# Kernel tuning notes

Measured on AMD Instinct MI355X. Metric: run time of the kernel, lower is better.

## Reference

```python
import jax, jax.numpy as jnp
import numpy as np

D_MODEL = 1024
N_HEADS = 16
D_K = D_MODEL // N_HEADS


def setup_inputs() -> dict:
    key = jax.random.key(0)
    kx, kq, kk, kv, ko = jax.random.split(key, 5)
    scale = 1.0 / np.sqrt(D_MODEL)
    return {
        "x": jax.random.normal(kx, (2, 2048, D_MODEL), dtype=jnp.float32),
        "W_Q": jax.random.normal(kq, (D_MODEL, D_MODEL), dtype=jnp.float32) * scale,
        "W_K": jax.random.normal(kk, (D_MODEL, D_MODEL), dtype=jnp.float32) * scale,
        "W_V": jax.random.normal(kv, (D_MODEL, D_MODEL), dtype=jnp.float32) * scale,
        "W_O": jax.random.normal(ko, (D_MODEL, D_MODEL), dtype=jnp.float32) * scale,
    }


def reference(x, W_Q, W_K, W_V, W_O) -> jnp.ndarray:
    B, S, _ = x.shape
    # Projections; weights stored as (d_model, d_model), applied as x @ W (Linear weight transposed convention folded into init)
    def heads(w):
        return jnp.einsum('bsd,de->bse', x, w).reshape(B, S, N_HEADS, D_K).transpose(0, 2, 1, 3)
    Q, K, V = heads(W_Q), heads(W_K), heads(W_V)  # (B,H,S,d_k)
    scores = jnp.einsum('bhqd,bhkd->bhqk', Q, K) / jnp.sqrt(jnp.asarray(D_K, x.dtype))
    causal_mask = jnp.triu(jnp.ones((S, S), dtype=bool), k=1)  # True above diagonal
    scores = jnp.where(causal_mask[None, None], jnp.asarray(-jnp.inf, x.dtype), scores)
    attn = jax.nn.softmax(scores, axis=-1)
    out = jnp.einsum('bhqk,bhkd->bhqd', attn, V)  # (B,H,S,d_k)
    out = out.transpose(0, 2, 1, 3).reshape(B, S, N_HEADS * D_K)
    return jnp.einsum('bsd,de->bse', out, W_O)
```

## Files before the change

kernel.cpp:

```cpp
#include <hip/hip_runtime.h>

typedef unsigned short u16;
typedef unsigned int u32;
typedef __attribute__((ext_vector_type(8))) __bf16 bf16x8;
typedef __attribute__((ext_vector_type(2))) __bf16 bf16x2;
typedef __attribute__((ext_vector_type(4))) float f32x4;
typedef __attribute__((ext_vector_type(16))) float f32x16;
typedef __attribute__((ext_vector_type(4))) u32 u32x4;

__device__ inline u16 f2bf(float f) {
  unsigned u = __builtin_bit_cast(unsigned, f);
  u += 0x7FFFu + ((u >> 16) & 1u);
  return (u16)(u >> 16);
}

__device__ inline u32 packbf(float a, float b) {
  bf16x2 t;
  t[0] = (__bf16)a;
  t[1] = (__bf16)b;
  return __builtin_bit_cast(u32, t);
}

__device__ inline void async16(const void* g, void* l) {
  __builtin_amdgcn_global_load_lds((const __attribute__((address_space(1))) void*)g,
                                   (__attribute__((address_space(3))) void*)l, 16, 0, 0);
}

__global__ __launch_bounds__(256) void xconv(const float* __restrict__ x, u16* __restrict__ xb) {
  int i = blockIdx.x * 256 + threadIdx.x;
  float4 v = ((const float4*)x)[i];
  ushort4 r;
  r.x = f2bf(v.x); r.y = f2bf(v.y); r.z = f2bf(v.z); r.w = f2bf(v.w);
  ((ushort4*)xb)[i] = r;
}

__global__ __launch_bounds__(256) void wtrans4(const float* __restrict__ W0,
                                               const float* __restrict__ W1,
                                               const float* __restrict__ W2,
                                               const float* __restrict__ W3,
                                               u16* __restrict__ WtQKV,
                                               u16* __restrict__ WtO) {
  __shared__ u16 tile[32][33];
  const int z = blockIdx.z;
  const float* W = (z == 0) ? W0 : (z == 1) ? W1 : (z == 2) ? W2 : W3;
  u16* Wt = (z < 3) ? (WtQKV + (size_t)z * 1024 * 1024) : WtO;
  const float s = (z == 0) ? 0.18033688011112042f : 1.0f;
  const int e0 = blockIdx.x * 32;
  const int d0 = blockIdx.y * 32;
  const int tx = threadIdx.x & 31;
  const int ty = threadIdx.x >> 5;
#pragma unroll
  for (int i = ty; i < 32; i += 8)
    tile[i][tx] = f2bf(W[(size_t)(d0 + i) * 1024 + e0 + tx] * s);
  __syncthreads();
#pragma unroll
  for (int i = ty; i < 32; i += 8)
    Wt[(size_t)(e0 + i) * 1024 + d0 + tx] = tile[tx][i];
}

__global__ __launch_bounds__(256) void vtrans(const u16* __restrict__ QKV, u16* __restrict__ Vtg) {
  __shared__ u16 t[32][66];
  const int tid = threadIdx.x;
  const int s0 = blockIdx.x * 32, dg0 = blockIdx.y * 64, b = blockIdx.z;
  {
    const int i = tid >> 3, c = (tid & 7) * 8;
    uint4 v = *(const uint4*)(QKV + (size_t)(b * 2048 + s0 + i) * 3072 + 2048 + dg0 + c);
    u16 tmp[8];
    *(uint4*)tmp = v;
#pragma unroll
    for (int e = 0; e < 8; ++e) t[i][c + e] = tmp[e];
  }
  __syncthreads();
  {
    const int r = tid >> 2, cg = (tid & 3) * 8;
    u16 tmp[8];
#pragma unroll
    for (int e = 0; e < 8; ++e) tmp[e] = t[cg + e][r];
    *(uint4*)(Vtg + (size_t)(b * 1024 + dg0 + r) * 2048 + s0 + cg) = *(uint4*)tmp;
  }
}

template <int OUT_BF16>
__global__ __launch_bounds__(256) void gemm_bt(const u16* __restrict__ A,
                                               const u16* __restrict__ Bt,
                                               void* __restrict__ Cp,
                                               int M, int N, int K) {
  __shared__ __align__(16) u16 As[128 * 32];
  __shared__ __align__(16) u16 Bs[128 * 32];
  const int tid = threadIdx.x;
  const int lane = tid & 63;
  const int wave = tid >> 6;
  const int lr = lane & 15;
  const int lk = (lane >> 4) * 8;
  const int wm = (wave >> 1) * 64;
  const int wn = (wave & 1) * 64;
  const int bm = blockIdx.x * 128;
  const int bn = blockIdx.y * 128;
  const int srow = lane >> 2;
  const int scol = (lane & 3) * 8;

  f32x4 acc[4][4] = {};

  for (int k0 = 0; k0 < K; k0 += 32) {
#pragma unroll
    for (int r = 0; r < 2; ++r) {
      const int chunk = r * 4 + wave;
      const int row = chunk * 16 + srow;
      async16(A + (size_t)(bm + row) * K + k0 + scol, &As[chunk * 512 + lane * 8]);
      async16(Bt + (size_t)(bn + row) * K + k0 + scol, &Bs[chunk * 512 + lane * 8]);
    }
    __syncthreads();
    bf16x8 a[4], b[4];
#pragma unroll
    for (int i = 0; i < 4; ++i) {
      a[i] = *(const bf16x8*)&As[(wm + i * 16 + lr) * 32 + lk];
      b[i] = *(const bf16x8*)&Bs[(wn + i * 16 + lr) * 32 + lk];
    }
#pragma unroll
    for (int mi = 0; mi < 4; ++mi)
#pragma unroll
      for (int ni = 0; ni < 4; ++ni)
        acc[mi][ni] = __builtin_amdgcn_mfma_f32_16x16x32_bf16(a[mi], b[ni], acc[mi][ni], 0, 0, 0);
    __syncthreads();
  }

#pragma unroll
  for (int mi = 0; mi < 4; ++mi) {
#pragma unroll
    for (int ni = 0; ni < 4; ++ni) {
      const int col = bn + wn + ni * 16 + lr;
#pragma unroll
      for (int j = 0; j < 4; ++j) {
        const int row = bm + wm + mi * 16 + (lane >> 4) * 4 + j;
        if (OUT_BF16)
          ((u16*)Cp)[(size_t)row * N + col] = f2bf(acc[mi][ni][j]);
        else
          ((float*)Cp)[(size_t)row * N + col] = acc[mi][ni][j];
      }
    }
  }
}

__global__ __launch_bounds__(256, 2) void attn_kernel(const u16* __restrict__ QKV,
                                                      const u16* __restrict__ Vtg,
                                                      u16* __restrict__ Opart,
                                                      float* __restrict__ Lpart) {
  constexpr int S = 2048, LD = 3072;
  constexpr float MFIX = 12.0f;
  __shared__ __align__(16) u16 Ks[2][64 * 64];
  __shared__ __align__(16) u16 Vs[2][64 * 64];

  const int g = 7 - (blockIdx.x >> 1);
  const int c = blockIdx.x & 1;
  const int bh = blockIdx.y;
  const int b = bh >> 4, h = bh & 15;
  const int tid = threadIdx.x, lane = tid & 63, w = tid >> 6;
  const int l31 = lane & 31, lh = lane >> 5;

  const int qbase = g * 256 + w * 64;
  const int ktlast = 4 * g + w;
  const int ktbeg = c * (2 * g + 2);
  const int ktend = (c + 1) * (2 * g + 2);

  bf16x8 qf[2][4];
#pragma unroll
  for (int qh = 0; qh < 2; ++qh) {
    const u16* qrow = QKV + (size_t)(b * S + qbase + qh * 32 + l31) * LD + h * 64;
#pragma unroll
    for (int cc = 0; cc < 4; ++cc) qf[qh][cc] = *(const bf16x8*)(qrow + cc * 16 + lh * 8);
  }

  const int c0 = tid, c1 = tid + 256;
  const int r0 = c0 >> 3, x0 = ((c0 & 7) ^ (r0 & 7)) << 3;
  const int r1 = c1 >> 3, x1 = ((c1 & 7) ^ (r1 & 7)) << 3;
  const u16* Kbase = QKV + (size_t)b * S * LD + 1024 + h * 64;
  const u16* Vbase = Vtg + (size_t)bh * 64 * 2048;

#define STAGE(buf, kt_)                                                          \
  do {                                                                           \
    async16(Kbase + (size_t)((kt_)*64 + r0) * LD + x0, &Ks[buf][c0 * 8]);        \
    async16(Kbase + (size_t)((kt_)*64 + r1) * LD + x1, &Ks[buf][c1 * 8]);        \
    async16(Vbase + (size_t)r0 * 2048 + (kt_)*64 + x0, &Vs[buf][c0 * 8]);        \
    async16(Vbase + (size_t)r1 * 2048 + (kt_)*64 + x1, &Vs[buf][c1 * 8]);        \
  } while (0)

  f32x16 o00 = {}, o01 = {}, o10 = {}, o11 = {};
  float l0 = 0.f, l1 = 0.f;

#define TREE16(dst, arr)                                                         \
  do {                                                                           \
    float v_[16];                                                                \
    _Pragma("unroll") for (int r_ = 0; r_ < 16; ++r_) v_[r_] = (arr)[r_];        \
    _Pragma("unroll") for (int s_ = 8; s_ >= 1; s_ >>= 1)                        \
      _Pragma("unroll") for (int r_ = 0; r_ < s_; ++r_) v_[r_] += v_[r_ + s_];   \
    dst += v_[0];                                                                \
  } while (0)

#define MAKE_PA(pa, pk, sw, q4)                                                  \
  bf16x8 pa;                                                                     \
  {                                                                              \
    u32x4 wv_;                                                                   \
    wv_[0] = lh ? (sw)[(q4) + 2] : (pk)[(q4) + 0];                               \
    wv_[1] = lh ? (sw)[(q4) + 3] : (pk)[(q4) + 1];                               \
    wv_[2] = lh ? (pk)[(q4) + 2] : (sw)[(q4) + 0];                               \
    wv_[3] = lh ? (pk)[(q4) + 3] : (sw)[(q4) + 1];                               \
    pa = __builtin_bit_cast(bf16x8, wv_);                                        \
  }

  STAGE(0, ktbeg);

  int cur = 0;
  for (int kt = ktbeg; kt < ktend; ++kt) {
    if (kt + 1 < ktend) {
      STAGE(cur ^ 1, kt + 1);
      asm volatile("s_waitcnt vmcnt(4)" ::: "memory");
    } else {
      asm volatile("s_waitcnt vmcnt(0)" ::: "memory");
    }
    __builtin_amdgcn_s_barrier();
    __builtin_amdgcn_sched_barrier(0);

    const bool active = (kt <= ktlast);
    if (active) {
      const bool full = (kt < ktlast);
      const u16* ks = Ks[cur];
      const u16* vs = Vs[cur];

      f32x16 t00 = {}, t10 = {}, t01 = {}, t11 = {};
      __builtin_amdgcn_s_setprio(1);
#pragma unroll
      for (int cc = 0; cc < 4; ++cc) {
        const int ci = 2 * cc + lh;
        const bf16x8 kf0 = *(const bf16x8*)&ks[l31 * 64 + ((ci ^ (l31 & 7)) << 3)];
        const bf16x8 kf1 = *(const bf16x8*)&ks[(32 + l31) * 64 + ((ci ^ (l31 & 7)) << 3)];
        t00 = __builtin_amdgcn_mfma_f32_32x32x16_bf16(kf0, qf[0][cc], t00, 0, 0, 0);
        t01 = __builtin_amdgcn_mfma_f32_32x32x16_bf16(kf0, qf[1][cc], t01, 0, 0, 0);
        if (full) t10 = __builtin_amdgcn_mfma_f32_32x32x16_bf16(kf1, qf[0][cc], t10, 0, 0, 0);
        t11 = __builtin_amdgcn_mfma_f32_32x32x16_bf16(kf1, qf[1][cc], t11, 0, 0, 0);
      }
      __builtin_amdgcn_s_setprio(0);

      if (!full) {
#pragma unroll
        for (int r = 0; r < 16; ++r) {
          const int ko = (r & 3) + 8 * (r >> 2) + 4 * lh;
          if (ko > l31) { t00[r] = -3e38f; t11[r] = -3e38f; }
        }
      }

      u32 pk0[8], pk1[8], sw0[8], sw1[8];

#pragma unroll
      for (int r = 0; r < 16; ++r) t00[r] = exp2f(t00[r] - MFIX);
#pragma unroll
      for (int r = 0; r < 16; ++r) t01[r] = exp2f(t01[r] - MFIX);
      TREE16(l0, t00);
      TREE16(l1, t01);
#pragma unroll
      for (int j = 0; j < 8; ++j) {
        pk0[j] = packbf(t00[2 * j], t00[2 * j + 1]);
        pk1[j] = packbf(t01[2 * j], t01[2 * j + 1]);
      }
#pragma unroll
      for (int j = 0; j < 8; ++j) {
        sw0[j] = __shfl_xor(pk0[j], 32);
        sw1[j] = __shfl_xor(pk1[j], 32);
      }
      __builtin_amdgcn_s_setprio(1);
#pragma unroll
      for (int kc = 0; kc < 2; ++kc) {
        const int q4 = kc * 4;
        MAKE_PA(pa0, pk0, sw0, q4)
        MAKE_PA(pa1, pk1, sw1, q4)
        const int ci = 2 * kc + lh;
        const bf16x8 vd0 = *(const bf16x8*)&vs[l31 * 64 + ((ci ^ (l31 & 7)) << 3)];
        const bf16x8 vd1 = *(const bf16x8*)&vs[(32 + l31) * 64 + ((ci ^ (l31 & 7)) << 3)];
        o00 = __builtin_amdgcn_mfma_f32_32x32x16_bf16(pa0, vd0, o00, 0, 0, 0);
        o01 = __builtin_amdgcn_mfma_f32_32x32x16_bf16(pa0, vd1, o01, 0, 0, 0);
        o10 = __builtin_amdgcn_mfma_f32_32x32x16_bf16(pa1, vd0, o10, 0, 0, 0);
        o11 = __builtin_amdgcn_mfma_f32_32x32x16_bf16(pa1, vd1, o11, 0, 0, 0);
      }
      __builtin_amdgcn_s_setprio(0);

      if (full) {
#pragma unroll
        for (int r = 0; r < 16; ++r) t10[r] = exp2f(t10[r] - MFIX);
        TREE16(l0, t10);
#pragma unroll
        for (int j = 0; j < 8; ++j) pk0[j] = packbf(t10[2 * j], t10[2 * j + 1]);
#pragma unroll
        for (int j = 0; j < 8; ++j) sw0[j] = __shfl_xor(pk0[j], 32);
      }
#pragma unroll
      for (int r = 0; r < 16; ++r) t11[r] = exp2f(t11[r] - MFIX);
      TREE16(l1, t11);
#pragma unroll
      for (int j = 0; j < 8; ++j) pk1[j] = packbf(t11[2 * j], t11[2 * j + 1]);
#pragma unroll
      for (int j = 0; j < 8; ++j) sw1[j] = __shfl_xor(pk1[j], 32);

      __builtin_amdgcn_s_setprio(1);
#pragma unroll
      for (int kc = 0; kc < 2; ++kc) {
        const int q4 = kc * 4;
        MAKE_PA(pa1, pk1, sw1, q4)
        const int ci = 2 * (kc + 2) + lh;
        const bf16x8 vd0 = *(const bf16x8*)&vs[l31 * 64 + ((ci ^ (l31 & 7)) << 3)];
        const bf16x8 vd1 = *(const bf16x8*)&vs[(32 + l31) * 64 + ((ci ^ (l31 & 7)) << 3)];
        if (full) {
          MAKE_PA(pa0, pk0, sw0, q4)
          o00 = __builtin_amdgcn_mfma_f32_32x32x16_bf16(pa0, vd0, o00, 0, 0, 0);
          o01 = __builtin_amdgcn_mfma_f32_32x32x16_bf16(pa0, vd1, o01, 0, 0, 0);
        }
        o10 = __builtin_amdgcn_mfma_f32_32x32x16_bf16(pa1, vd0, o10, 0, 0, 0);
        o11 = __builtin_amdgcn_mfma_f32_32x32x16_bf16(pa1, vd1, o11, 0, 0, 0);
      }
      __builtin_amdgcn_s_setprio(0);
    }

    asm volatile("s_waitcnt lgkmcnt(0)" ::: "memory");
    __builtin_amdgcn_s_barrier();
    cur ^= 1;
  }
#undef STAGE
#undef TREE16
#undef MAKE_PA

  const float l0t = l0 + __shfl_xor(l0, 32);
  const float l1t = l1 + __shfl_xor(l1, 32);
  u16* Oc = Opart + (size_t)c * 4096 * 1024;
#pragma unroll
  for (int r = 0; r < 16; ++r) {
    const int qo = (r & 3) + 8 * (r >> 2) + 4 * lh;
    u16* p0 = Oc + (size_t)(b * S + qbase + qo) * 1024 + h * 64 + l31;
    u16* p1 = p0 + (size_t)32 * 1024;
    p0[0] = f2bf(o00[r]);
    p0[32] = f2bf(o01[r]);
    p1[0] = f2bf(o10[r]);
    p1[32] = f2bf(o11[r]);
  }
  if (lh == 0) {
    Lpart[(size_t)c * 4096 * 16 + (size_t)(b * S + qbase + l31) * 16 + h] = l0t;
    Lpart[(size_t)c * 4096 * 16 + (size_t)(b * S + qbase + 32 + l31) * 16 + h] = l1t;
  }
}

__global__ __launch_bounds__(256) void combine(const u16* __restrict__ Opart,
                                               const float* __restrict__ Lpart,
                                               u16* __restrict__ Obuf) {
  const int i = blockIdx.x * 256 + threadIdx.x;
  const int row = i >> 7;
  const int cw = (i & 127) * 8;
  const int h = cw >> 6;
  const float l = Lpart[(size_t)row * 16 + h] + Lpart[(size_t)4096 * 16 + (size_t)row * 16 + h];
  const float inv = 1.0f / l;
  const bf16x8 a = *(const bf16x8*)(Opart + (size_t)row * 1024 + cw);
  const bf16x8 bq = *(const bf16x8*)(Opart + (size_t)4096 * 1024 + (size_t)row * 1024 + cw);
  u16 out[8];
#pragma unroll
  for (int j = 0; j < 8; ++j) out[j] = f2bf(((float)a[j] + (float)bq[j]) * inv);
  *(uint4*)(Obuf + (size_t)row * 1024 + cw) = *(uint4*)out;
}

extern "C" void kernel_launch(void* const* d_in, const int* in_sizes, int n_in,
                              void* d_out, int out_size, void* d_ws, size_t ws_size,
                              hipStream_t stream) {
  const float* x  = (const float*)d_in[0];
  const float* WQ = (const float*)d_in[1];
  const float* WK = (const float*)d_in[2];
  const float* WV = (const float*)d_in[3];
  const float* WO = (const float*)d_in[4];
  float* out = (float*)d_out;

  u16* xb    = (u16*)d_ws;
  u16* WtQKV = xb + (size_t)4096 * 1024;
  u16* WtO   = WtQKV + (size_t)3072 * 1024;
  u16* QKV   = WtO + (size_t)1024 * 1024;
  u16* Obuf  = QKV + (size_t)4096 * 3072;
  u16* Vtg   = Obuf + (size_t)4096 * 1024;
  u16* Opart = Vtg + (size_t)2048 * 2048;
  float* Lpart = (float*)(Opart + (size_t)2 * 4096 * 1024);

  xconv<<<4096, 256, 0, stream>>>(x, xb);
  wtrans4<<<dim3(32, 32, 4), 256, 0, stream>>>(WQ, WK, WV, WO, WtQKV, WtO);

  gemm_bt<1><<<dim3(32, 24), 256, 0, stream>>>(xb, WtQKV, QKV, 4096, 3072, 1024);
  vtrans<<<dim3(64, 16, 2), 256, 0, stream>>>(QKV, Vtg);
  attn_kernel<<<dim3(16, 32), 256, 0, stream>>>(QKV, Vtg, Opart, Lpart);
  combine<<<2048, 256, 0, stream>>>(Opart, Lpart, Obuf);
  gemm_bt<0><<<dim3(32, 8), 256, 0, stream>>>(Obuf, WtO, out, 4096, 1024, 1024);
}
```

Measured before the change: 147.5 us.

## Load V tiles directly into registers and drop the LDS V buffer

V tiles are no longer staged through shared memory. Each wave now loads its V fragments straight from global memory into a register double buffer (current and next tile), with the vmcnt wait adjusted so it retires only the current tile's loads. This halves LDS use, removes the V LDS reads, and raises the launch-bounds occupancy target from 2 to 3 blocks. In exchange, every wave re-fetches the same V tile from global/cache, and the extra register buffers under a tighter register budget risk spills or lower effective occupancy.

New measurement: 413.8 us. 2.81x slower.

```diff
diff --git a/kernel.cpp b/kernel.cpp
--- a/kernel.cpp
+++ b/kernel.cpp
@@ -141,14 +141,13 @@
   }
 }
 
-__global__ __launch_bounds__(256, 2) void attn_kernel(const u16* __restrict__ QKV,
+__global__ __launch_bounds__(256, 3) void attn_kernel(const u16* __restrict__ QKV,
                                                       const u16* __restrict__ Vtg,
                                                       u16* __restrict__ Opart,
                                                       float* __restrict__ Lpart) {
   constexpr int S = 2048, LD = 3072;
   constexpr float MFIX = 12.0f;
   __shared__ __align__(16) u16 Ks[2][64 * 64];
-  __shared__ __align__(16) u16 Vs[2][64 * 64];
 
   const int g = 7 - (blockIdx.x >> 1);
   const int c = blockIdx.x & 1;
@@ -174,14 +173,22 @@
   const int r0 = c0 >> 3, x0 = ((c0 & 7) ^ (r0 & 7)) << 3;
   const int r1 = c1 >> 3, x1 = ((c1 & 7) ^ (r1 & 7)) << 3;
   const u16* Kbase = QKV + (size_t)b * S * LD + 1024 + h * 64;
-  const u16* Vbase = Vtg + (size_t)bh * 64 * 2048;
-
-#define STAGE(buf, kt_)                                                          \
+  const u16* Vr0 = Vtg + (size_t)(bh * 64 + l31) * 2048;
+  const u16* Vr1 = Vtg + (size_t)(bh * 64 + 32 + l31) * 2048;
+
+#define STAGEK(buf, kt_)                                                         \
   do {                                                                           \
     async16(Kbase + (size_t)((kt_)*64 + r0) * LD + x0, &Ks[buf][c0 * 8]);        \
     async16(Kbase + (size_t)((kt_)*64 + r1) * LD + x1, &Ks[buf][c1 * 8]);        \
-    async16(Vbase + (size_t)r0 * 2048 + (kt_)*64 + x0, &Vs[buf][c0 * 8]);        \
-    async16(Vbase + (size_t)r1 * 2048 + (kt_)*64 + x1, &Vs[buf][c1 * 8]);        \
+  } while (0)
+
+#define VLOAD(d0_, d1_, kt_)                                                     \
+  do {                                                                           \
+    _Pragma("unroll") for (int kc = 0; kc < 4; ++kc) {                           \
+      const int ci = 2 * kc + lh;                                                \
+      d0_[kc] = *(const bf16x8*)(Vr0 + (kt_)*64 + ci * 8);                       \
+      d1_[kc] = *(const bf16x8*)(Vr1 + (kt_)*64 + ci * 8);                       \
+    }                                                                            \
   } while (0)
 
   f32x16 o00 = {}, o01 = {}, o10 = {}, o11 = {};
@@ -207,13 +214,18 @@
     pa = __builtin_bit_cast(bf16x8, wv_);                                        \
   }
 
-  STAGE(0, ktbeg);
+  bf16x8 vc0[4], vc1[4], vn0[4], vn1[4];
+
+  STAGEK(0, ktbeg);
+  VLOAD(vc0, vc1, ktbeg);
 
   int cur = 0;
   for (int kt = ktbeg; kt < ktend; ++kt) {
     if (kt + 1 < ktend) {
-      STAGE(cur ^ 1, kt + 1);
-      asm volatile("s_waitcnt vmcnt(4)" ::: "memory");
+      STAGEK(cur ^ 1, kt + 1);
+      VLOAD(vn0, vn1, kt + 1);
+      __builtin_amdgcn_sched_barrier(0);
+      asm volatile("s_waitcnt vmcnt(10)" ::: "memory");
     } else {
       asm volatile("s_waitcnt vmcnt(0)" ::: "memory");
     }
@@ -224,7 +236,6 @@
     if (active) {
       const bool full = (kt < ktlast);
       const u16* ks = Ks[cur];
-      const u16* vs = Vs[cur];
 
       f32x16 t00 = {}, t10 = {}, t01 = {}, t11 = {};
       __builtin_amdgcn_s_setprio(1);
@@ -272,13 +283,10 @@
         const int q4 = kc * 4;
         MAKE_PA(pa0, pk0, sw0, q4)
         MAKE_PA(pa1, pk1, sw1, q4)
-        const int ci = 2 * kc + lh;
-        const bf16x8 vd0 = *(const bf16x8*)&vs[l31 * 64 + ((ci ^ (l31 & 7)) << 3)];
-        const bf16x8 vd1 = *(const bf16x8*)&vs[(32 + l31) * 64 + ((ci ^ (l31 & 7)) << 3)];
-        o00 = __builtin_amdgcn_mfma_f32_32x32x16_bf16(pa0, vd0, o00, 0, 0, 0);
-        o01 = __builtin_amdgcn_mfma_f32_32x32x16_bf16(pa0, vd1, o01, 0, 0, 0);
-        o10 = __builtin_amdgcn_mfma_f32_32x32x16_bf16(pa1, vd0, o10, 0, 0, 0);
-        o11 = __builtin_amdgcn_mfma_f32_32x32x16_bf16(pa1, vd1, o11, 0, 0, 0);
+        o00 = __builtin_amdgcn_mfma_f32_32x32x16_bf16(pa0, vc0[kc], o00, 0, 0, 0);
+        o01 = __builtin_amdgcn_mfma_f32_32x32x16_bf16(pa0, vc1[kc], o01, 0, 0, 0);
+        o10 = __builtin_amdgcn_mfma_f32_32x32x16_bf16(pa1, vc0[kc], o10, 0, 0, 0);
+        o11 = __builtin_amdgcn_mfma_f32_32x32x16_bf16(pa1, vc1[kc], o11, 0, 0, 0);
       }
       __builtin_amdgcn_s_setprio(0);
 
@@ -304,25 +312,28 @@
       for (int kc = 0; kc < 2; ++kc) {
         const int q4 = kc * 4;
         MAKE_PA(pa1, pk1, sw1, q4)
-        const int ci = 2 * (kc + 2) + lh;
-        const bf16x8 vd0 = *(const bf16x8*)&vs[l31 * 64 + ((ci ^ (l31 & 7)) << 3)];
-        const bf16x8 vd1 = *(const bf16x8*)&vs[(32 + l31) * 64 + ((ci ^ (l31 & 7)) << 3)];
         if (full) {
           MAKE_PA(pa0, pk0, sw0, q4)
-          o00 = __builtin_amdgcn_mfma_f32_32x32x16_bf16(pa0, vd0, o00, 0, 0, 0);
-          o01 = __builtin_amdgcn_mfma_f32_32x32x16_bf16(pa0, vd1, o01, 0, 0, 0);
+          o00 = __builtin_amdgcn_mfma_f32_32x32x16_bf16(pa0, vc0[kc + 2], o00, 0, 0, 0);
+          o01 = __builtin_amdgcn_mfma_f32_32x32x16_bf16(pa0, vc1[kc + 2], o01, 0, 0, 0);
         }
-        o10 = __builtin_amdgcn_mfma_f32_32x32x16_bf16(pa1, vd0, o10, 0, 0, 0);
-        o11 = __builtin_amdgcn_mfma_f32_32x32x16_bf16(pa1, vd1, o11, 0, 0, 0);
+        o10 = __builtin_amdgcn_mfma_f32_32x32x16_bf16(pa1, vc0[kc + 2], o10, 0, 0, 0);
+        o11 = __builtin_amdgcn_mfma_f32_32x32x16_bf16(pa1, vc1[kc + 2], o11, 0, 0, 0);
       }
       __builtin_amdgcn_s_setprio(0);
     }
 
+#pragma unroll
+    for (int kc = 0; kc < 4; ++kc) {
+      vc0[kc] = vn0[kc];
+      vc1[kc] = vn1[kc];
+    }
     asm volatile("s_waitcnt lgkmcnt(0)" ::: "memory");
     __builtin_amdgcn_s_barrier();
     cur ^= 1;
   }
-#undef STAGE
+#undef STAGEK
+#undef VLOAD
 #undef TREE16
 #undef MAKE_PA
 
```

## Permute V sequence order in transpose to drop P-matrix cross-lane shuffles

Applied to the files above, without the earlier changes.

The V transpose kernel now writes keys within each group of 16 in a permuted order, swapping bits 2 and 3 of the sequence index. The permutation is chosen to match the register layout of the exponentiated score tiles, so the P operand can be packed straight from each lane's own values. This removes the 32-lane xor shuffles and selects from the attention inner loop. Correctness depends on the permutation exactly matching the MFMA accumulator-to-operand layout.

After: 140.6 us. -4.7%, faster.

```diff
diff --git a/kernel.cpp b/kernel.cpp
--- a/kernel.cpp
+++ b/kernel.cpp
@@ -75,7 +75,11 @@
     const int r = tid >> 2, cg = (tid & 3) * 8;
     u16 tmp[8];
 #pragma unroll
-    for (int e = 0; e < 8; ++e) tmp[e] = t[cg + e][r];
+    for (int e = 0; e < 8; ++e) {
+      const int x = cg + e;
+      const int sx = (x & ~12) | ((x & 4) << 1) | ((x & 8) >> 1);
+      tmp[e] = t[sx][r];
+    }
     *(uint4*)(Vtg + (size_t)(b * 1024 + dg0 + r) * 2048 + s0 + cg) = *(uint4*)tmp;
   }
 }
@@ -196,14 +200,14 @@
     dst += v_[0];                                                                \
   } while (0)
 
-#define MAKE_PA(pa, pk, sw, q4)                                                  \
+#define MAKE_PA(pa, pk, q4)                                                      \
   bf16x8 pa;                                                                     \
   {                                                                              \
     u32x4 wv_;                                                                   \
-    wv_[0] = lh ? (sw)[(q4) + 2] : (pk)[(q4) + 0];                               \
-    wv_[1] = lh ? (sw)[(q4) + 3] : (pk)[(q4) + 1];                               \
-    wv_[2] = lh ? (pk)[(q4) + 2] : (sw)[(q4) + 0];                               \
-    wv_[3] = lh ? (pk)[(q4) + 3] : (sw)[(q4) + 1];                               \
+    wv_[0] = (pk)[(q4) + 0];                                                     \
+    wv_[1] = (pk)[(q4) + 1];                                                     \
+    wv_[2] = (pk)[(q4) + 2];                                                     \
+    wv_[3] = (pk)[(q4) + 3];                                                     \
     pa = __builtin_bit_cast(bf16x8, wv_);                                        \
   }
 
@@ -248,7 +252,7 @@
         }
       }
 
-      u32 pk0[8], pk1[8], sw0[8], sw1[8];
+      u32 pk0[8], pk1[8];
 
 #pragma unroll
       for (int r = 0; r < 16; ++r) t00[r] = exp2f(t00[r] - MFIX);
@@ -261,17 +265,12 @@
         pk0[j] = packbf(t00[2 * j], t00[2 * j + 1]);
         pk1[j] = packbf(t01[2 * j], t01[2 * j + 1]);
       }
-#pragma unroll
-      for (int j = 0; j < 8; ++j) {
-        sw0[j] = __shfl_xor(pk0[j], 32);
-        sw1[j] = __shfl_xor(pk1[j], 32);
-      }
       __builtin_amdgcn_s_setprio(1);
 #pragma unroll
       for (int kc = 0; kc < 2; ++kc) {
         const int q4 = kc * 4;
-        MAKE_PA(pa0, pk0, sw0, q4)
-        MAKE_PA(pa1, pk1, sw1, q4)
+        MAKE_PA(pa0, pk0, q4)
+        MAKE_PA(pa1, pk1, q4)
         const int ci = 2 * kc + lh;
         const bf16x8 vd0 = *(const bf16x8*)&vs[l31 * 64 + ((ci ^ (l31 & 7)) << 3)];
         const bf16x8 vd1 = *(const bf16x8*)&vs[(32 + l31) * 64 + ((ci ^ (l31 & 7)) << 3)];
@@ -288,27 +287,23 @@
         TREE16(l0, t10);
 #pragma unroll
         for (int j = 0; j < 8; ++j) pk0[j] = packbf(t10[2 * j], t10[2 * j + 1]);
-#pragma unroll
-        for (int j = 0; j < 8; ++j) sw0[j] = __shfl_xor(pk0[j], 32);
       }
 #pragma unroll
       for (int r = 0; r < 16; ++r) t11[r] = exp2f(t11[r] - MFIX);
       TREE16(l1, t11);
 #pragma unroll
       for (int j = 0; j < 8; ++j) pk1[j] = packbf(t11[2 * j], t11[2 * j + 1]);
-#pragma unroll
-      for (int j = 0; j < 8; ++j) sw1[j] = __shfl_xor(pk1[j], 32);
 
       __builtin_amdgcn_s_setprio(1);
 #pragma unroll
       for (int kc = 0; kc < 2; ++kc) {
         const int q4 = kc * 4;
-        MAKE_PA(pa1, pk1, sw1, q4)
+        MAKE_PA(pa1, pk1, q4)
         const int ci = 2 * (kc + 2) + lh;
         const bf16x8 vd0 = *(const bf16x8*)&vs[l31 * 64 + ((ci ^ (l31 & 7)) << 3)];
         const bf16x8 vd1 = *(const bf16x8*)&vs[(32 + l31) * 64 + ((ci ^ (l31 & 7)) << 3)];
         if (full) {
-          MAKE_PA(pa0, pk0, sw0, q4)
+          MAKE_PA(pa0, pk0, q4)
           o00 = __builtin_amdgcn_mfma_f32_32x32x16_bf16(pa0, vd0, o00, 0, 0, 0);
           o01 = __builtin_amdgcn_mfma_f32_32x32x16_bf16(pa0, vd1, o01, 0, 0, 0);
         }
```
